# Kernel optimization log

Measured on AMD Instinct MI355X. Metric: run time of the kernel, lower is better.

Reference implementation:

```python
import jax, jax.numpy as jnp
import numpy as np

E, D_IN, H, D_OUT = 8, 6, 32, 2
B = 1048576

def setup_inputs() -> dict:
    key = jax.random.key(0)
    ks = jax.random.split(key, 11)
    s = lambda *sh: 1.0 / np.sqrt(sh[-2])  # glorot-ish scale
    x = jax.random.normal(ks[0], (B, D_IN), dtype=jnp.float32)
    # stacked expert weights
    W1 = jax.random.normal(ks[1], (E, D_IN, H), dtype=jnp.float32) * (1.0/np.sqrt(D_IN))
    b1 = jnp.zeros((E, H), dtype=jnp.float32)
    W2 = jax.random.normal(ks[2], (E, H, H), dtype=jnp.float32) * (1.0/np.sqrt(H))
    b2 = jnp.zeros((E, H), dtype=jnp.float32)
    W3 = jax.random.normal(ks[3], (E, H, D_OUT), dtype=jnp.float32) * (1.0/np.sqrt(H))
    b3 = jnp.zeros((E, D_OUT), dtype=jnp.float32)
    # gating network
    Wg1 = jax.random.normal(ks[4], (D_IN, H), dtype=jnp.float32) * (1.0/np.sqrt(D_IN))
    bg1 = jnp.zeros((H,), dtype=jnp.float32)
    Wg2 = jax.random.normal(ks[5], (H, E), dtype=jnp.float32) * (1.0/np.sqrt(H))
    bg2 = jnp.zeros((E,), dtype=jnp.float32)
    return {"x": x, "W1": W1, "b1": b1, "W2": W2, "b2": b2, "W3": W3, "b3": b3,
            "Wg1": Wg1, "bg1": bg1, "Wg2": Wg2, "bg2": bg2}

def reference(x, W1, b1, W2, b2, W3, b3, Wg1, bg1, Wg2, bg2):
    # gate: [B, E] softmax probs
    g = jax.nn.softmax(jax.nn.relu(x @ Wg1 + bg1) @ Wg2 + bg2, axis=-1)
    # all experts as batched GEMMs: h1, h2 [B, E, H]; y [B, E, 2]
    h1 = jax.nn.relu(jnp.einsum('bd,edh->beh', x, W1) + b1)
    h2 = jax.nn.relu(jnp.einsum('beh,ehk->bek', h1, W2) + b2)
    y = jnp.einsum('beh,eho->beo', h2, W3) + b3
    # gate-weighted sum over experts -> [B, 2]
    return jnp.einsum('be,beo->bo', g, y)
```

## Files before the change

kernel.cpp:

```cpp
#include <hip/hip_runtime.h>


typedef _Float16 half2_t __attribute__((ext_vector_type(2)));
typedef _Float16 half4_t __attribute__((ext_vector_type(4)));
typedef _Float16 half8_t __attribute__((ext_vector_type(8)));
typedef __fp16   fp16v2  __attribute__((ext_vector_type(2)));
typedef float  float4_t __attribute__((ext_vector_type(4)));
typedef float  float2_t __attribute__((ext_vector_type(2)));
typedef int    int2_t   __attribute__((ext_vector_type(2)));
typedef int    int4_t   __attribute__((ext_vector_type(4)));

#define MFMA_K32(A, B, C) __builtin_amdgcn_mfma_f32_16x16x32_f16((A), (B), (C), 0, 0, 0)
#define MFMA_K16(A, B, C) __builtin_amdgcn_mfma_f32_16x16x16f16((A), (B), (C), 0, 0, 0)

static constexpr int E_ = 8, DIN_ = 6, H_ = 32, EPW_ = 2;

union H8U { half2_t h2[4]; half8_t h8; int4_t i4; };
union H4U { half2_t h2[2]; half4_t h4; int2_t i2; };
union HI  { half2_t h; int i; };
union PKU { fp16v2 p; half2_t h; };
union FI  { float f; int i; };

__device__ __forceinline__ half2_t pkrtz(float a, float b) {
    PKU u; u.p = __builtin_amdgcn_cvt_pkrtz(a, b);
    return u.h;
}

__device__ __forceinline__ half2_t relu2(half2_t v) {
    const half2_t z = {(_Float16)0.0f, (_Float16)0.0f};
    return __builtin_elementwise_max(v, z);
}

__device__ __forceinline__ float bperm_f(int addr, float v) {
    FI u; u.f = v;
    u.i = __builtin_amdgcn_ds_bpermute(addr, u.i);
    return u.f;
}

__global__ __launch_bounds__(256, 2)
void moe_kernel(
    const float* __restrict__ x,  const float* __restrict__ W1, const float* __restrict__ b1,
    const float* __restrict__ W2, const float* __restrict__ b2, const float* __restrict__ W3,
    const float* __restrict__ b3, const float* __restrict__ Wg1, const float* __restrict__ bg1,
    const float* __restrict__ Wg2, const float* __restrict__ bg2,
    float* __restrict__ out, int nTiles, int tilesPerBlock)
{
    const int tid  = threadIdx.x;
    const int lane = tid & 63;
    const int t    = lane & 15;
    const int q    = lane >> 4;
    const int wv   = tid >> 6;
    const int eb   = wv * EPW_;

    __shared__ float2_t cbuf[2][4][16];

    const float L2E = 1.44269504f;

    H4U G1[2];
    #pragma unroll
    for (int f = 0; f < 2; ++f) {
        float v0 = 0.f, v1 = 0.f, v2 = 0.f, v3 = 0.f;
        if (q == 0) {
            v0 = Wg1[0 * H_ + f * 16 + t]; v1 = Wg1[1 * H_ + f * 16 + t];
            v2 = Wg1[2 * H_ + f * 16 + t]; v3 = Wg1[3 * H_ + f * 16 + t];
        } else if (q == 1) {
            v0 = Wg1[4 * H_ + f * 16 + t]; v1 = Wg1[5 * H_ + f * 16 + t];
            v2 = bg1[f * 16 + t];          v3 = 0.f;
        }
        G1[f].h2[0] = pkrtz(v0, v1); G1[f].h2[1] = pkrtz(v2, v3);
    }
    H8U G2;
    #pragma unroll
    for (int p = 0; p < 4; ++p) {
        int c0 = ((p >> 1) << 4) + q * 4 + ((p & 1) << 1);
        float v0 = (t < E_) ? Wg2[c0 * E_ + t] * L2E : 0.f;
        float v1 = (t < E_) ? Wg2[(c0 + 1) * E_ + t] * L2E : 0.f;
        G2.h2[p] = pkrtz(v0, v1);
    }

    H4U W1F[EPW_][2];
    H8U W2F[EPW_][2], W3F[EPW_], B2R[EPW_];
    #pragma unroll
    for (int j = 0; j < EPW_; ++j) {
        const int e = eb + j;
        #pragma unroll
        for (int f = 0; f < 2; ++f) {
            float v0 = 0.f, v1 = 0.f, v2 = 0.f, v3 = 0.f;
            const float* We = W1 + (size_t)e * DIN_ * H_ + f * 16 + t;
            if (q == 0)      { v0 = We[0 * H_]; v1 = We[1 * H_]; v2 = We[2 * H_]; v3 = We[3 * H_]; }
            else if (q == 1) { v0 = We[4 * H_]; v1 = We[5 * H_]; v2 = b1[e * H_ + f * 16 + t]; }
            W1F[j][f].h2[0] = pkrtz(v0, v1); W1F[j][f].h2[1] = pkrtz(v2, v3);
        }
        #pragma unroll
        for (int p = 0; p < 4; ++p) {
            int c0 = ((p >> 1) << 4) + q * 4 + ((p & 1) << 1);
            W2F[j][0].h2[p] = pkrtz(W2[(e * H_ + c0) * H_ + 0  + t], W2[(e * H_ + c0 + 1) * H_ + 0  + t]);
            W2F[j][1].h2[p] = pkrtz(W2[(e * H_ + c0) * H_ + 16 + t], W2[(e * H_ + c0 + 1) * H_ + 16 + t]);
            B2R[j].h2[p]    = pkrtz(b2[e * H_ + c0], b2[e * H_ + c0 + 1]);
            float v0 = 0.f, v1 = 0.f;
            if ((t >> 1) == e) {
                v0 = W3[(e * H_ + c0) * 2 + (t & 1)];
                v1 = W3[(e * H_ + c0 + 1) * 2 + (t & 1)];
            }
            W3F[j].h2[p] = pkrtz(v0, v1);
        }
    }

    float4_t bg2F, b3F;
    #pragma unroll
    for (int r = 0; r < 4; ++r) {
        int m = q * 4 + r;
        bg2F[r] = (m < E_) ? bg2[m] * L2E : 0.f;
        b3F[r]  = b3[m];
    }
    const float4_t zero4 = {0.f, 0.f, 0.f, 0.f};

    const int gsrc = ((((q >> 1) << 4) | t) << 2);
    const int csrc = (((wv << 4) | t) << 2);

    const int tile0 = blockIdx.x * tilesPerBlock;

    const int xo1 = (q == 0) ? 0 : 4;
    const int xo2 = (q == 0) ? 2 : 4;
    const float* xq = x + ((size_t)tile0 * 16 + t) * DIN_;
    float2_t la = {0.f, 0.f}, lb = {0.f, 0.f};
    if (tile0 < nTiles) {
        la = *(const float2_t*)(xq + xo1);
        lb = *(const float2_t*)(xq + xo2);
    }

    HI onei; onei.h = pkrtz(1.f, 0.f);
    const bool isq0 = (q == 0);

    for (int it = 0; it < tilesPerBlock; ++it) {
        const int tile = tile0 + it;
        if (tile >= nTiles) break;

        H4U ux;
        ux.h2[0] = pkrtz(la[0], la[1]);
        HI hb; hb.h = pkrtz(lb[0], lb[1]);
        HI se; se.i = isq0 ? hb.i : onei.i;
        ux.h2[1] = se.h;
        const half4_t xB = ux.h4;

        if ((it + 1) < tilesPerBlock && (tile + 1) < nTiles) {
            const float* xn = xq + (size_t)(it + 1) * 16 * DIN_;
            la = *(const float2_t*)(xn + xo1);
            lb = *(const float2_t*)(xn + xo2);
        }

        float4_t hgLo = MFMA_K16(G1[0].h4, xB, zero4);
        float4_t hgHi = MFMA_K16(G1[1].h4, xB, zero4);
        H8U uh;
        uh.h2[0] = relu2(pkrtz(hgLo[0], hgLo[1]));
        uh.h2[1] = relu2(pkrtz(hgLo[2], hgLo[3]));
        uh.h2[2] = relu2(pkrtz(hgHi[0], hgHi[1]));
        uh.h2[3] = relu2(pkrtz(hgHi[2], hgHi[3]));
        float4_t gl = MFMA_K32(G2.h8, uh.h8, bg2F);

        float ex0 = __builtin_amdgcn_exp2f(gl[0]);
        float ex1 = __builtin_amdgcn_exp2f(gl[1]);
        float ex2 = __builtin_amdgcn_exp2f(gl[2]);
        float ex3 = __builtin_amdgcn_exp2f(gl[3]);
        float s = (ex0 + ex1) + (ex2 + ex3);
        s += __shfl_xor(s, 16);
        float rs = __builtin_amdgcn_rcpf(s);
        HI pa, pb;
        pa.h = pkrtz(ex0, ex1);
        pb.h = pkrtz(ex2, ex3);
        int va = __builtin_amdgcn_ds_bpermute(gsrc, pa.i);
        int vb = __builtin_amdgcn_ds_bpermute(gsrc, pb.i);
        HI gsel; gsel.i = (q & 1) ? vb : va;
        float ga = (float)gsel.h[0];
        float gb = (float)gsel.h[1];

        float4_t Y = b3F;
        #pragma unroll
        for (int j = 0; j < EPW_; ++j) {
            float4_t lo = MFMA_K16(W1F[j][0].h4, xB, zero4);
            float4_t hi = MFMA_K16(W1F[j][1].h4, xB, zero4);
            H8U u1;
            u1.h2[0] = relu2(pkrtz(lo[0], lo[1]));
            u1.h2[1] = relu2(pkrtz(lo[2], lo[3]));
            u1.h2[2] = relu2(pkrtz(hi[0], hi[1]));
            u1.h2[3] = relu2(pkrtz(hi[2], hi[3]));
            float4_t lo2 = MFMA_K32(W2F[j][0].h8, u1.h8, zero4);
            float4_t hi2 = MFMA_K32(W2F[j][1].h8, u1.h8, zero4);
            H8U u2;
            u2.h2[0] = relu2(pkrtz(lo2[0], lo2[1]) + B2R[j].h2[0]);
            u2.h2[1] = relu2(pkrtz(lo2[2], lo2[3]) + B2R[j].h2[1]);
            u2.h2[2] = relu2(pkrtz(hi2[0], hi2[1]) + B2R[j].h2[2]);
            u2.h2[3] = relu2(pkrtz(hi2[2], hi2[3]) + B2R[j].h2[3]);
            Y = MFMA_K32(W3F[j].h8, u2.h8, Y);
        }

        float p0 = ga * Y[0] + gb * Y[2];
        float p1 = ga * Y[1] + gb * Y[3];
        p0 = bperm_f(csrc, p0);
        p1 = bperm_f(csrc, p1);

        if (lane < 16) {
            float2_t o = {p0, p1};
            cbuf[it & 1][wv][t] = o;
        }
        __syncthreads();
        if (wv == 0 && lane < 16) {
            float2_t o  = cbuf[it & 1][0][t];
            float2_t o1 = cbuf[it & 1][1][t];
            float2_t o2 = cbuf[it & 1][2][t];
            float2_t o3 = cbuf[it & 1][3][t];
            o[0] = (o[0] + o1[0] + o2[0] + o3[0]) * rs;
            o[1] = (o[1] + o1[1] + o2[1] + o3[1]) * rs;
            *(float2_t*)(out + ((size_t)tile * 16 + t) * 2) = o;
        }
    }
}

extern "C" void kernel_launch(void* const* d_in, const int* in_sizes, int n_in,
                              void* d_out, int out_size, void* d_ws, size_t ws_size,
                              hipStream_t stream) {
    const float* x   = (const float*)d_in[0];
    const float* W1  = (const float*)d_in[1];
    const float* b1  = (const float*)d_in[2];
    const float* W2  = (const float*)d_in[3];
    const float* b2  = (const float*)d_in[4];
    const float* W3  = (const float*)d_in[5];
    const float* b3  = (const float*)d_in[6];
    const float* Wg1 = (const float*)d_in[7];
    const float* bg1 = (const float*)d_in[8];
    const float* Wg2 = (const float*)d_in[9];
    const float* bg2 = (const float*)d_in[10];
    float* out = (float*)d_out;

    const int B      = in_sizes[0] / DIN_;
    const int nTiles = (B + 15) / 16;
    const int blocks = 2048;
    const int tpb    = (nTiles + blocks - 1) / blocks;

    moe_kernel<<<blocks, 256, 0, stream>>>(x, W1, b1, W2, b2, W3, b3,
                                           Wg1, bg1, Wg2, bg2, out, nTiles, tpb);
}
```

Before: 155.3 us.

## Switch MoE tile pipeline to 32x32x16 MFMA with 32-row tiles

Reworks every GEMM stage (gate and expert layers) from 16x16 MFMA shapes to 32x32x16 f16 MFMAs that process 32 batch rows per tile. The fragment layouts, the gate softmax exchange (now a cross-half shuffle) and the output reduction are rewritten to match. The b2 bias moves to packed shared memory and the b3 bias is folded in after gating. The aim is fewer MFMA and conversion instructions per row and less per-tile sync overhead. The cost is larger accumulators, more register pressure, and half as many blocks.

After: 163.2 us. 5.1% more time.

```diff
diff --git a/kernel.cpp b/kernel.cpp
--- a/kernel.cpp
+++ b/kernel.cpp
@@ -2,24 +2,19 @@
 
 
 typedef _Float16 half2_t __attribute__((ext_vector_type(2)));
-typedef _Float16 half4_t __attribute__((ext_vector_type(4)));
 typedef _Float16 half8_t __attribute__((ext_vector_type(8)));
 typedef __fp16   fp16v2  __attribute__((ext_vector_type(2)));
-typedef float  float4_t __attribute__((ext_vector_type(4)));
-typedef float  float2_t __attribute__((ext_vector_type(2)));
-typedef int    int2_t   __attribute__((ext_vector_type(2)));
-typedef int    int4_t   __attribute__((ext_vector_type(4)));
-
-#define MFMA_K32(A, B, C) __builtin_amdgcn_mfma_f32_16x16x32_f16((A), (B), (C), 0, 0, 0)
-#define MFMA_K16(A, B, C) __builtin_amdgcn_mfma_f32_16x16x16f16((A), (B), (C), 0, 0, 0)
+typedef float  float2_t  __attribute__((ext_vector_type(2)));
+typedef float  float16_t __attribute__((ext_vector_type(16)));
+typedef int    int4_t    __attribute__((ext_vector_type(4)));
+
+#define MFMA32(A, B, C) __builtin_amdgcn_mfma_f32_32x32x16_f16((A), (B), (C), 0, 0, 0)
 
 static constexpr int E_ = 8, DIN_ = 6, H_ = 32, EPW_ = 2;
 
 union H8U { half2_t h2[4]; half8_t h8; int4_t i4; };
-union H4U { half2_t h2[2]; half4_t h4; int2_t i2; };
 union HI  { half2_t h; int i; };
 union PKU { fp16v2 p; half2_t h; };
-union FI  { float f; int i; };
 
 __device__ __forceinline__ half2_t pkrtz(float a, float b) {
     PKU u; u.p = __builtin_amdgcn_cvt_pkrtz(a, b);
@@ -31,13 +26,11 @@
     return __builtin_elementwise_max(v, z);
 }
 
-__device__ __forceinline__ float bperm_f(int addr, float v) {
-    FI u; u.f = v;
-    u.i = __builtin_amdgcn_ds_bpermute(addr, u.i);
-    return u.f;
-}
-
-__global__ __launch_bounds__(256, 2)
+__device__ __forceinline__ int sigma(int p, int h, int j) {
+    return (j & 3) + 8 * ((j >> 2) + 2 * p) + 4 * h;
+}
+
+__global__ __launch_bounds__(256)
 void moe_kernel(
     const float* __restrict__ x,  const float* __restrict__ W1, const float* __restrict__ b1,
     const float* __restrict__ W2, const float* __restrict__ b2, const float* __restrict__ W3,
@@ -47,171 +40,195 @@
 {
     const int tid  = threadIdx.x;
     const int lane = tid & 63;
-    const int t    = lane & 15;
-    const int q    = lane >> 4;
+    const int t32  = lane & 31;
+    const int h    = lane >> 5;
     const int wv   = tid >> 6;
     const int eb   = wv * EPW_;
 
-    __shared__ float2_t cbuf[2][4][16];
+    __shared__ int      b2pk[128];
+    __shared__ float2_t cbuf[2][4][32];
 
     const float L2E = 1.44269504f;
 
-    H4U G1[2];
-    #pragma unroll
-    for (int f = 0; f < 2; ++f) {
-        float v0 = 0.f, v1 = 0.f, v2 = 0.f, v3 = 0.f;
-        if (q == 0) {
-            v0 = Wg1[0 * H_ + f * 16 + t]; v1 = Wg1[1 * H_ + f * 16 + t];
-            v2 = Wg1[2 * H_ + f * 16 + t]; v3 = Wg1[3 * H_ + f * 16 + t];
-        } else if (q == 1) {
-            v0 = Wg1[4 * H_ + f * 16 + t]; v1 = Wg1[5 * H_ + f * 16 + t];
-            v2 = bg1[f * 16 + t];          v3 = 0.f;
-        }
-        G1[f].h2[0] = pkrtz(v0, v1); G1[f].h2[1] = pkrtz(v2, v3);
-    }
-    H8U G2;
-    #pragma unroll
-    for (int p = 0; p < 4; ++p) {
-        int c0 = ((p >> 1) << 4) + q * 4 + ((p & 1) << 1);
-        float v0 = (t < E_) ? Wg2[c0 * E_ + t] * L2E : 0.f;
-        float v1 = (t < E_) ? Wg2[(c0 + 1) * E_ + t] * L2E : 0.f;
-        G2.h2[p] = pkrtz(v0, v1);
-    }
-
-    H4U W1F[EPW_][2];
-    H8U W2F[EPW_][2], W3F[EPW_], B2R[EPW_];
-    #pragma unroll
-    for (int j = 0; j < EPW_; ++j) {
-        const int e = eb + j;
-        #pragma unroll
-        for (int f = 0; f < 2; ++f) {
-            float v0 = 0.f, v1 = 0.f, v2 = 0.f, v3 = 0.f;
-            const float* We = W1 + (size_t)e * DIN_ * H_ + f * 16 + t;
-            if (q == 0)      { v0 = We[0 * H_]; v1 = We[1 * H_]; v2 = We[2 * H_]; v3 = We[3 * H_]; }
-            else if (q == 1) { v0 = We[4 * H_]; v1 = We[5 * H_]; v2 = b1[e * H_ + f * 16 + t]; }
-            W1F[j][f].h2[0] = pkrtz(v0, v1); W1F[j][f].h2[1] = pkrtz(v2, v3);
-        }
-        #pragma unroll
-        for (int p = 0; p < 4; ++p) {
-            int c0 = ((p >> 1) << 4) + q * 4 + ((p & 1) << 1);
-            W2F[j][0].h2[p] = pkrtz(W2[(e * H_ + c0) * H_ + 0  + t], W2[(e * H_ + c0 + 1) * H_ + 0  + t]);
-            W2F[j][1].h2[p] = pkrtz(W2[(e * H_ + c0) * H_ + 16 + t], W2[(e * H_ + c0 + 1) * H_ + 16 + t]);
-            B2R[j].h2[p]    = pkrtz(b2[e * H_ + c0], b2[e * H_ + c0 + 1]);
+    if (tid < 128) {
+        int e = tid >> 4, hh = (tid >> 3) & 1, s = tid & 7;
+        int r0 = ((2 * s) & 3) + 8 * (s >> 1) + 4 * hh;
+        HI u; u.h = pkrtz(b2[e * H_ + r0], b2[e * H_ + r0 + 1]);
+        b2pk[tid] = u.i;
+    }
+    __syncthreads();
+
+    const int m = t32;
+
+    H8U G1;
+    #pragma unroll
+    for (int r = 0; r < 4; ++r) {
+        int j0 = 2 * r, j1 = 2 * r + 1;
+        float v0 = 0.f, v1 = 0.f;
+        if (h == 0) {
+            v0 = (j0 < DIN_) ? Wg1[j0 * H_ + m] : ((j0 == DIN_) ? bg1[m] : 0.f);
+            v1 = (j1 < DIN_) ? Wg1[j1 * H_ + m] : ((j1 == DIN_) ? bg1[m] : 0.f);
+        }
+        G1.h2[r] = pkrtz(v0, v1);
+    }
+    H8U Gg2[2];
+    #pragma unroll
+    for (int p = 0; p < 2; ++p)
+        #pragma unroll
+        for (int r = 0; r < 4; ++r) {
+            int c0 = sigma(p, h, 2 * r);
+            float v0 = (m < E_) ? Wg2[c0 * E_ + m] * L2E : 0.f;
+            float v1 = (m < E_) ? Wg2[(c0 + 1) * E_ + m] * L2E : 0.f;
+            Gg2[p].h2[r] = pkrtz(v0, v1);
+        }
+
+    H8U A1[EPW_], A2[EPW_][2], A3[EPW_][2];
+    #pragma unroll
+    for (int jx = 0; jx < EPW_; ++jx) {
+        const int e = eb + jx;
+        #pragma unroll
+        for (int r = 0; r < 4; ++r) {
+            int j0 = 2 * r, j1 = 2 * r + 1;
             float v0 = 0.f, v1 = 0.f;
-            if ((t >> 1) == e) {
-                v0 = W3[(e * H_ + c0) * 2 + (t & 1)];
-                v1 = W3[(e * H_ + c0 + 1) * 2 + (t & 1)];
-            }
-            W3F[j].h2[p] = pkrtz(v0, v1);
-        }
-    }
-
-    float4_t bg2F, b3F;
+            if (h == 0) {
+                v0 = (j0 < DIN_) ? W1[(e * DIN_ + j0) * H_ + m] : ((j0 == DIN_) ? b1[e * H_ + m] : 0.f);
+                v1 = (j1 < DIN_) ? W1[(e * DIN_ + j1) * H_ + m] : ((j1 == DIN_) ? b1[e * H_ + m] : 0.f);
+            }
+            A1[jx].h2[r] = pkrtz(v0, v1);
+        }
+        #pragma unroll
+        for (int p = 0; p < 2; ++p)
+            #pragma unroll
+            for (int r = 0; r < 4; ++r) {
+                int c0 = sigma(p, h, 2 * r);
+                A2[jx][p].h2[r] = pkrtz(W2[(e * H_ + c0) * H_ + m], W2[(e * H_ + c0 + 1) * H_ + m]);
+            }
+        const bool mine = (m >> 1) == e;
+        const int  o    = m & 1;
+        #pragma unroll
+        for (int p = 0; p < 2; ++p)
+            #pragma unroll
+            for (int r = 0; r < 4; ++r) {
+                int c0 = sigma(p, h, 2 * r);
+                float v0 = mine ? W3[(e * H_ + c0) * 2 + o] : 0.f;
+                float v1 = mine ? W3[(e * H_ + c0 + 1) * 2 + o] : 0.f;
+                A3[jx][p].h2[r] = pkrtz(v0, v1);
+            }
+    }
+
+    float bg2F[4], b3A[4], b3B[4];
     #pragma unroll
     for (int r = 0; r < 4; ++r) {
-        int m = q * 4 + r;
-        bg2F[r] = (m < E_) ? bg2[m] * L2E : 0.f;
-        b3F[r]  = b3[m];
-    }
-    const float4_t zero4 = {0.f, 0.f, 0.f, 0.f};
-
-    const int gsrc = ((((q >> 1) << 4) | t) << 2);
-    const int csrc = (((wv << 4) | t) << 2);
+        bg2F[r] = bg2[r + 4 * h] * L2E;
+        b3A[r]  = b3[4 * h + r];
+        b3B[r]  = b3[8 + 4 * h + r];
+    }
+    const float16_t zero16 = {0.f,0.f,0.f,0.f, 0.f,0.f,0.f,0.f, 0.f,0.f,0.f,0.f, 0.f,0.f,0.f,0.f};
 
     const int tile0 = blockIdx.x * tilesPerBlock;
 
-    const int xo1 = (q == 0) ? 0 : 4;
-    const int xo2 = (q == 0) ? 2 : 4;
-    const float* xq = x + ((size_t)tile0 * 16 + t) * DIN_;
-    float2_t la = {0.f, 0.f}, lb = {0.f, 0.f};
+    const float* xq = x + ((size_t)tile0 * 32 + t32) * DIN_;
+    float2_t la = {0.f, 0.f}, lb = {0.f, 0.f}, lc = {0.f, 0.f};
     if (tile0 < nTiles) {
-        la = *(const float2_t*)(xq + xo1);
-        lb = *(const float2_t*)(xq + xo2);
-    }
-
-    HI onei; onei.h = pkrtz(1.f, 0.f);
-    const bool isq0 = (q == 0);
+        la = *(const float2_t*)(xq + 0);
+        lb = *(const float2_t*)(xq + 2);
+        lc = *(const float2_t*)(xq + 4);
+    }
+    HI one0; one0.h = pkrtz(1.f, 0.f);
 
     for (int it = 0; it < tilesPerBlock; ++it) {
         const int tile = tile0 + it;
         if (tile >= nTiles) break;
 
-        H4U ux;
+        H8U ux;
         ux.h2[0] = pkrtz(la[0], la[1]);
-        HI hb; hb.h = pkrtz(lb[0], lb[1]);
-        HI se; se.i = isq0 ? hb.i : onei.i;
-        ux.h2[1] = se.h;
-        const half4_t xB = ux.h4;
+        ux.h2[1] = pkrtz(lb[0], lb[1]);
+        ux.h2[2] = pkrtz(lc[0], lc[1]);
+        ux.h2[3] = one0.h;
+        const half8_t xB = ux.h8;
 
         if ((it + 1) < tilesPerBlock && (tile + 1) < nTiles) {
-            const float* xn = xq + (size_t)(it + 1) * 16 * DIN_;
-            la = *(const float2_t*)(xn + xo1);
-            lb = *(const float2_t*)(xn + xo2);
-        }
-
-        float4_t hgLo = MFMA_K16(G1[0].h4, xB, zero4);
-        float4_t hgHi = MFMA_K16(G1[1].h4, xB, zero4);
-        H8U uh;
-        uh.h2[0] = relu2(pkrtz(hgLo[0], hgLo[1]));
-        uh.h2[1] = relu2(pkrtz(hgLo[2], hgLo[3]));
-        uh.h2[2] = relu2(pkrtz(hgHi[0], hgHi[1]));
-        uh.h2[3] = relu2(pkrtz(hgHi[2], hgHi[3]));
-        float4_t gl = MFMA_K32(G2.h8, uh.h8, bg2F);
-
-        float ex0 = __builtin_amdgcn_exp2f(gl[0]);
-        float ex1 = __builtin_amdgcn_exp2f(gl[1]);
-        float ex2 = __builtin_amdgcn_exp2f(gl[2]);
-        float ex3 = __builtin_amdgcn_exp2f(gl[3]);
+            const float* xn = xq + (size_t)(it + 1) * 32 * DIN_;
+            la = *(const float2_t*)(xn + 0);
+            lb = *(const float2_t*)(xn + 2);
+            lc = *(const float2_t*)(xn + 4);
+        }
+
+        float16_t Cg = MFMA32(G1.h8, xB, zero16);
+        H8U bg0, bg1v;
+        #pragma unroll
+        for (int r = 0; r < 4; ++r) {
+            bg0.h2[r]  = relu2(pkrtz(Cg[2 * r], Cg[2 * r + 1]));
+            bg1v.h2[r] = relu2(pkrtz(Cg[8 + 2 * r], Cg[9 + 2 * r]));
+        }
+        float16_t Cg2 = MFMA32(Gg2[0].h8, bg0.h8, zero16);
+        Cg2 = MFMA32(Gg2[1].h8, bg1v.h8, Cg2);
+
+        float ex0 = __builtin_amdgcn_exp2f(Cg2[0] + bg2F[0]);
+        float ex1 = __builtin_amdgcn_exp2f(Cg2[1] + bg2F[1]);
+        float ex2 = __builtin_amdgcn_exp2f(Cg2[2] + bg2F[2]);
+        float ex3 = __builtin_amdgcn_exp2f(Cg2[3] + bg2F[3]);
         float s = (ex0 + ex1) + (ex2 + ex3);
-        s += __shfl_xor(s, 16);
+        s += __shfl_xor(s, 32);
         float rs = __builtin_amdgcn_rcpf(s);
-        HI pa, pb;
+        HI pa, pb, xpa, xpb, eA, eB;
         pa.h = pkrtz(ex0, ex1);
         pb.h = pkrtz(ex2, ex3);
-        int va = __builtin_amdgcn_ds_bpermute(gsrc, pa.i);
-        int vb = __builtin_amdgcn_ds_bpermute(gsrc, pb.i);
-        HI gsel; gsel.i = (q & 1) ? vb : va;
-        float ga = (float)gsel.h[0];
-        float gb = (float)gsel.h[1];
-
-        float4_t Y = b3F;
-        #pragma unroll
-        for (int j = 0; j < EPW_; ++j) {
-            float4_t lo = MFMA_K16(W1F[j][0].h4, xB, zero4);
-            float4_t hi = MFMA_K16(W1F[j][1].h4, xB, zero4);
-            H8U u1;
-            u1.h2[0] = relu2(pkrtz(lo[0], lo[1]));
-            u1.h2[1] = relu2(pkrtz(lo[2], lo[3]));
-            u1.h2[2] = relu2(pkrtz(hi[0], hi[1]));
-            u1.h2[3] = relu2(pkrtz(hi[2], hi[3]));
-            float4_t lo2 = MFMA_K32(W2F[j][0].h8, u1.h8, zero4);
-            float4_t hi2 = MFMA_K32(W2F[j][1].h8, u1.h8, zero4);
-            H8U u2;
-            u2.h2[0] = relu2(pkrtz(lo2[0], lo2[1]) + B2R[j].h2[0]);
-            u2.h2[1] = relu2(pkrtz(lo2[2], lo2[3]) + B2R[j].h2[1]);
-            u2.h2[2] = relu2(pkrtz(hi2[0], hi2[1]) + B2R[j].h2[2]);
-            u2.h2[3] = relu2(pkrtz(hi2[2], hi2[3]) + B2R[j].h2[3]);
-            Y = MFMA_K32(W3F[j].h8, u2.h8, Y);
-        }
-
-        float p0 = ga * Y[0] + gb * Y[2];
-        float p1 = ga * Y[1] + gb * Y[3];
-        p0 = bperm_f(csrc, p0);
-        p1 = bperm_f(csrc, p1);
-
-        if (lane < 16) {
+        xpa.i = __shfl_xor(pa.i, 32);
+        xpb.i = __shfl_xor(pb.i, 32);
+        eA.i = h ? xpb.i : pa.i;
+        eB.i = h ? pb.i  : xpa.i;
+        float gA0 = (float)eA.h[0], gA1 = (float)eA.h[1];
+        float gB0 = (float)eB.h[0], gB1 = (float)eB.h[1];
+
+        float16_t Y = zero16;
+        #pragma unroll
+        for (int jx = 0; jx < EPW_; ++jx) {
+            float16_t C1 = MFMA32(A1[jx].h8, xB, zero16);
+            H8U u0, u1;
+            #pragma unroll
+            for (int r = 0; r < 4; ++r) {
+                u0.h2[r] = relu2(pkrtz(C1[2 * r], C1[2 * r + 1]));
+                u1.h2[r] = relu2(pkrtz(C1[8 + 2 * r], C1[9 + 2 * r]));
+            }
+            float16_t C2 = MFMA32(A2[jx][0].h8, u0.h8, zero16);
+            C2 = MFMA32(A2[jx][1].h8, u1.h8, C2);
+            H8U ua, ub;
+            const int base = (eb + jx) * 16 + h * 8;
+            ua.i4 = *(const int4_t*)&b2pk[base];
+            ub.i4 = *(const int4_t*)&b2pk[base + 4];
+            H8U q0, q1;
+            #pragma unroll
+            for (int r = 0; r < 4; ++r) {
+                q0.h2[r] = relu2(pkrtz(C2[2 * r], C2[2 * r + 1]) + ua.h2[r]);
+                q1.h2[r] = relu2(pkrtz(C2[8 + 2 * r], C2[9 + 2 * r]) + ub.h2[r]);
+            }
+            Y = MFMA32(A3[jx][0].h8, q0.h8, Y);
+            Y = MFMA32(A3[jx][1].h8, q1.h8, Y);
+        }
+
+        float p0 = gA0 * Y[0] + gA1 * Y[2] + gB0 * Y[4] + gB1 * Y[6];
+        float p1 = gA0 * Y[1] + gA1 * Y[3] + gB0 * Y[5] + gB1 * Y[7];
+        if (wv == 0) {
+            p0 += gA0 * b3A[0] + gA1 * b3A[2] + gB0 * b3B[0] + gB1 * b3B[2];
+            p1 += gA0 * b3A[1] + gA1 * b3A[3] + gB0 * b3B[1] + gB1 * b3B[3];
+        }
+        p0 += __shfl_xor(p0, 32);
+        p1 += __shfl_xor(p1, 32);
+
+        if (lane < 32) {
             float2_t o = {p0, p1};
-            cbuf[it & 1][wv][t] = o;
+            cbuf[it & 1][wv][t32] = o;
         }
         __syncthreads();
-        if (wv == 0 && lane < 16) {
-            float2_t o  = cbuf[it & 1][0][t];
-            float2_t o1 = cbuf[it & 1][1][t];
-            float2_t o2 = cbuf[it & 1][2][t];
-            float2_t o3 = cbuf[it & 1][3][t];
+        if (wv == 0 && lane < 32) {
+            float2_t o  = cbuf[it & 1][0][t32];
+            float2_t o1 = cbuf[it & 1][1][t32];
+            float2_t o2 = cbuf[it & 1][2][t32];
+            float2_t o3 = cbuf[it & 1][3][t32];
             o[0] = (o[0] + o1[0] + o2[0] + o3[0]) * rs;
             o[1] = (o[1] + o1[1] + o2[1] + o3[1]) * rs;
-            *(float2_t*)(out + ((size_t)tile * 16 + t) * 2) = o;
+            *(float2_t*)(out + ((size_t)tile * 32 + t32) * 2) = o;
         }
     }
 }
@@ -233,8 +250,8 @@
     float* out = (float*)d_out;
 
     const int B      = in_sizes[0] / DIN_;
-    const int nTiles = (B + 15) / 16;
-    const int blocks = 2048;
+    const int nTiles = (B + 31) / 32;
+    const int blocks = 1024;
     const int tpb    = (nTiles + blocks - 1) / blocks;
 
     moe_kernel<<<blocks, 256, 0, stream>>>(x, W1, b1, W2, b2, W3, b3,
```

## Process two tiles per iteration to interleave independent MFMA chains

Applied to the files above, without the earlier changes.

The per-tile loop is unrolled by two. The gating and expert MFMA chains of the two tiles are interleaved so their latencies can overlap, and the two results share one shared-memory reduction and one __syncthreads. The minimum-occupancy hint is also removed from the launch bounds, which lets the compiler use more registers for the doubled live state. The risks are higher register pressure and lower occupancy, and, if tilesPerBlock is odd, redundant work and writes to a tile that belongs to the next block.

Result: slower. 166.4 us (+7.1%).

```diff
diff --git a/kernel.cpp b/kernel.cpp
--- a/kernel.cpp
+++ b/kernel.cpp
@@ -37,7 +37,7 @@
     return u.f;
 }
 
-__global__ __launch_bounds__(256, 2)
+__global__ __launch_bounds__(256)
 void moe_kernel(
     const float* __restrict__ x,  const float* __restrict__ W1, const float* __restrict__ b1,
     const float* __restrict__ W2, const float* __restrict__ b2, const float* __restrict__ W3,
@@ -52,7 +52,7 @@
     const int wv   = tid >> 6;
     const int eb   = wv * EPW_;
 
-    __shared__ float2_t cbuf[2][4][16];
+    __shared__ float2_t cbuf[2][2][4][16];
 
     const float L2E = 1.44269504f;
 
@@ -123,95 +123,150 @@
     const int xo1 = (q == 0) ? 0 : 4;
     const int xo2 = (q == 0) ? 2 : 4;
     const float* xq = x + ((size_t)tile0 * 16 + t) * DIN_;
-    float2_t la = {0.f, 0.f}, lb = {0.f, 0.f};
-    if (tile0 < nTiles) {
-        la = *(const float2_t*)(xq + xo1);
-        lb = *(const float2_t*)(xq + xo2);
-    }
+    const int strideT = 16 * DIN_;
+
+    float2_t laA = {0.f,0.f}, lbA = {0.f,0.f}, laB = {0.f,0.f}, lbB = {0.f,0.f};
+    if (tile0 < nTiles)     { laA = *(const float2_t*)(xq + xo1);           lbA = *(const float2_t*)(xq + xo2); }
+    if (tile0 + 1 < nTiles) { laB = *(const float2_t*)(xq + strideT + xo1); lbB = *(const float2_t*)(xq + strideT + xo2); }
 
     HI onei; onei.h = pkrtz(1.f, 0.f);
     const bool isq0 = (q == 0);
 
-    for (int it = 0; it < tilesPerBlock; ++it) {
-        const int tile = tile0 + it;
-        if (tile >= nTiles) break;
-
-        H4U ux;
-        ux.h2[0] = pkrtz(la[0], la[1]);
-        HI hb; hb.h = pkrtz(lb[0], lb[1]);
-        HI se; se.i = isq0 ? hb.i : onei.i;
-        ux.h2[1] = se.h;
-        const half4_t xB = ux.h4;
-
-        if ((it + 1) < tilesPerBlock && (tile + 1) < nTiles) {
-            const float* xn = xq + (size_t)(it + 1) * 16 * DIN_;
-            la = *(const float2_t*)(xn + xo1);
-            lb = *(const float2_t*)(xn + xo2);
-        }
-
-        float4_t hgLo = MFMA_K16(G1[0].h4, xB, zero4);
-        float4_t hgHi = MFMA_K16(G1[1].h4, xB, zero4);
-        H8U uh;
-        uh.h2[0] = relu2(pkrtz(hgLo[0], hgLo[1]));
-        uh.h2[1] = relu2(pkrtz(hgLo[2], hgLo[3]));
-        uh.h2[2] = relu2(pkrtz(hgHi[0], hgHi[1]));
-        uh.h2[3] = relu2(pkrtz(hgHi[2], hgHi[3]));
-        float4_t gl = MFMA_K32(G2.h8, uh.h8, bg2F);
-
-        float ex0 = __builtin_amdgcn_exp2f(gl[0]);
-        float ex1 = __builtin_amdgcn_exp2f(gl[1]);
-        float ex2 = __builtin_amdgcn_exp2f(gl[2]);
-        float ex3 = __builtin_amdgcn_exp2f(gl[3]);
-        float s = (ex0 + ex1) + (ex2 + ex3);
-        s += __shfl_xor(s, 16);
-        float rs = __builtin_amdgcn_rcpf(s);
-        HI pa, pb;
-        pa.h = pkrtz(ex0, ex1);
-        pb.h = pkrtz(ex2, ex3);
-        int va = __builtin_amdgcn_ds_bpermute(gsrc, pa.i);
-        int vb = __builtin_amdgcn_ds_bpermute(gsrc, pb.i);
-        HI gsel; gsel.i = (q & 1) ? vb : va;
-        float ga = (float)gsel.h[0];
-        float gb = (float)gsel.h[1];
-
-        float4_t Y = b3F;
+    for (int it = 0; it < tilesPerBlock; it += 2) {
+        const int tA = tile0 + it;
+        if (tA >= nTiles) break;
+        const int  tB   = tA + 1;
+        const bool hasB = (tB < nTiles);
+
+        H4U uxA, uxB;
+        {
+            uxA.h2[0] = pkrtz(laA[0], laA[1]);
+            HI hb; hb.h = pkrtz(lbA[0], lbA[1]);
+            HI se; se.i = isq0 ? hb.i : onei.i;
+            uxA.h2[1] = se.h;
+            uxB.h2[0] = pkrtz(laB[0], laB[1]);
+            HI hb2; hb2.h = pkrtz(lbB[0], lbB[1]);
+            HI se2; se2.i = isq0 ? hb2.i : onei.i;
+            uxB.h2[1] = se2.h;
+        }
+        const half4_t xBA = uxA.h4;
+        const half4_t xBB = uxB.h4;
+
+        if ((it + 2) < tilesPerBlock) {
+            const float* xn = xq + (size_t)(it + 2) * strideT;
+            if (tA + 2 < nTiles) { laA = *(const float2_t*)(xn + xo1);           lbA = *(const float2_t*)(xn + xo2); }
+            if (tA + 3 < nTiles) { laB = *(const float2_t*)(xn + strideT + xo1); lbB = *(const float2_t*)(xn + strideT + xo2); }
+        }
+
+        float4_t glA, glB;
+        {
+            float4_t hgLo = MFMA_K16(G1[0].h4, xBA, zero4);
+            float4_t hgHi = MFMA_K16(G1[1].h4, xBA, zero4);
+            float4_t hgLo2 = MFMA_K16(G1[0].h4, xBB, zero4);
+            float4_t hgHi2 = MFMA_K16(G1[1].h4, xBB, zero4);
+            H8U uh, uh2;
+            uh.h2[0] = relu2(pkrtz(hgLo[0], hgLo[1]));
+            uh.h2[1] = relu2(pkrtz(hgLo[2], hgLo[3]));
+            uh.h2[2] = relu2(pkrtz(hgHi[0], hgHi[1]));
+            uh.h2[3] = relu2(pkrtz(hgHi[2], hgHi[3]));
+            uh2.h2[0] = relu2(pkrtz(hgLo2[0], hgLo2[1]));
+            uh2.h2[1] = relu2(pkrtz(hgLo2[2], hgLo2[3]));
+            uh2.h2[2] = relu2(pkrtz(hgHi2[0], hgHi2[1]));
+            uh2.h2[3] = relu2(pkrtz(hgHi2[2], hgHi2[3]));
+            glA = MFMA_K32(G2.h8, uh.h8, bg2F);
+            glB = MFMA_K32(G2.h8, uh2.h8, bg2F);
+        }
+
+        float exA0 = __builtin_amdgcn_exp2f(glA[0]);
+        float exA1 = __builtin_amdgcn_exp2f(glA[1]);
+        float exA2 = __builtin_amdgcn_exp2f(glA[2]);
+        float exA3 = __builtin_amdgcn_exp2f(glA[3]);
+        float exB0 = __builtin_amdgcn_exp2f(glB[0]);
+        float exB1 = __builtin_amdgcn_exp2f(glB[1]);
+        float exB2 = __builtin_amdgcn_exp2f(glB[2]);
+        float exB3 = __builtin_amdgcn_exp2f(glB[3]);
+        float sA = (exA0 + exA1) + (exA2 + exA3);
+        float sB = (exB0 + exB1) + (exB2 + exB3);
+        sA += __shfl_xor(sA, 16);
+        sB += __shfl_xor(sB, 16);
+        float rsA = __builtin_amdgcn_rcpf(sA);
+        float rsB = __builtin_amdgcn_rcpf(sB);
+        HI paA, pbA, paB, pbB;
+        paA.h = pkrtz(exA0, exA1);  pbA.h = pkrtz(exA2, exA3);
+        paB.h = pkrtz(exB0, exB1);  pbB.h = pkrtz(exB2, exB3);
+        int vaA = __builtin_amdgcn_ds_bpermute(gsrc, paA.i);
+        int vbA = __builtin_amdgcn_ds_bpermute(gsrc, pbA.i);
+        int vaB = __builtin_amdgcn_ds_bpermute(gsrc, paB.i);
+        int vbB = __builtin_amdgcn_ds_bpermute(gsrc, pbB.i);
+        HI gsA; gsA.i = (q & 1) ? vbA : vaA;
+        HI gsB; gsB.i = (q & 1) ? vbB : vaB;
+        float gaA = (float)gsA.h[0], gbA = (float)gsA.h[1];
+        float gaB = (float)gsB.h[0], gbB = (float)gsB.h[1];
+
+        float4_t YA = b3F, YB = b3F;
         #pragma unroll
         for (int j = 0; j < EPW_; ++j) {
-            float4_t lo = MFMA_K16(W1F[j][0].h4, xB, zero4);
-            float4_t hi = MFMA_K16(W1F[j][1].h4, xB, zero4);
-            H8U u1;
-            u1.h2[0] = relu2(pkrtz(lo[0], lo[1]));
-            u1.h2[1] = relu2(pkrtz(lo[2], lo[3]));
-            u1.h2[2] = relu2(pkrtz(hi[0], hi[1]));
-            u1.h2[3] = relu2(pkrtz(hi[2], hi[3]));
-            float4_t lo2 = MFMA_K32(W2F[j][0].h8, u1.h8, zero4);
-            float4_t hi2 = MFMA_K32(W2F[j][1].h8, u1.h8, zero4);
-            H8U u2;
-            u2.h2[0] = relu2(pkrtz(lo2[0], lo2[1]) + B2R[j].h2[0]);
-            u2.h2[1] = relu2(pkrtz(lo2[2], lo2[3]) + B2R[j].h2[1]);
-            u2.h2[2] = relu2(pkrtz(hi2[0], hi2[1]) + B2R[j].h2[2]);
-            u2.h2[3] = relu2(pkrtz(hi2[2], hi2[3]) + B2R[j].h2[3]);
-            Y = MFMA_K32(W3F[j].h8, u2.h8, Y);
-        }
-
-        float p0 = ga * Y[0] + gb * Y[2];
-        float p1 = ga * Y[1] + gb * Y[3];
-        p0 = bperm_f(csrc, p0);
-        p1 = bperm_f(csrc, p1);
-
-        if (lane < 16) {
-            float2_t o = {p0, p1};
-            cbuf[it & 1][wv][t] = o;
+            float4_t loA = MFMA_K16(W1F[j][0].h4, xBA, zero4);
+            float4_t hiA = MFMA_K16(W1F[j][1].h4, xBA, zero4);
+            float4_t loB = MFMA_K16(W1F[j][0].h4, xBB, zero4);
+            float4_t hiB = MFMA_K16(W1F[j][1].h4, xBB, zero4);
+            H8U u1A, u1B;
+            u1A.h2[0] = relu2(pkrtz(loA[0], loA[1]));
+            u1A.h2[1] = relu2(pkrtz(loA[2], loA[3]));
+            u1A.h2[2] = relu2(pkrtz(hiA[0], hiA[1]));
+            u1A.h2[3] = relu2(pkrtz(hiA[2], hiA[3]));
+            u1B.h2[0] = relu2(pkrtz(loB[0], loB[1]));
+            u1B.h2[1] = relu2(pkrtz(loB[2], loB[3]));
+            u1B.h2[2] = relu2(pkrtz(hiB[0], hiB[1]));
+            u1B.h2[3] = relu2(pkrtz(hiB[2], hiB[3]));
+            float4_t lo2A = MFMA_K32(W2F[j][0].h8, u1A.h8, zero4);
+            float4_t hi2A = MFMA_K32(W2F[j][1].h8, u1A.h8, zero4);
+            float4_t lo2B = MFMA_K32(W2F[j][0].h8, u1B.h8, zero4);
+            float4_t hi2B = MFMA_K32(W2F[j][1].h8, u1B.h8, zero4);
+            H8U u2A, u2B;
+            u2A.h2[0] = relu2(pkrtz(lo2A[0], lo2A[1]) + B2R[j].h2[0]);
+            u2A.h2[1] = relu2(pkrtz(lo2A[2], lo2A[3]) + B2R[j].h2[1]);
+            u2A.h2[2] = relu2(pkrtz(hi2A[0], hi2A[1]) + B2R[j].h2[2]);
+            u2A.h2[3] = relu2(pkrtz(hi2A[2], hi2A[3]) + B2R[j].h2[3]);
+            u2B.h2[0] = relu2(pkrtz(lo2B[0], lo2B[1]) + B2R[j].h2[0]);
+            u2B.h2[1] = relu2(pkrtz(lo2B[2], lo2B[3]) + B2R[j].h2[1]);
+            u2B.h2[2] = relu2(pkrtz(hi2B[0], hi2B[1]) + B2R[j].h2[2]);
+            u2B.h2[3] = relu2(pkrtz(hi2B[2], hi2B[3]) + B2R[j].h2[3]);
+            YA = MFMA_K32(W3F[j].h8, u2A.h8, YA);
+            YB = MFMA_K32(W3F[j].h8, u2B.h8, YB);
+        }
+
+        float pA0 = gaA * YA[0] + gbA * YA[2];
+        float pA1 = gaA * YA[1] + gbA * YA[3];
+        float pB0 = gaB * YB[0] + gbB * YB[2];
+        float pB1 = gaB * YB[1] + gbB * YB[3];
+        pA0 = bperm_f(csrc, pA0);
+        pA1 = bperm_f(csrc, pA1);
+        pB0 = bperm_f(csrc, pB0);
+        pB1 = bperm_f(csrc, pB1);
+
+        const int par = (it >> 1) & 1;
+        if (lane < 32) {
+            const int sel = lane >> 4;
+            float2_t o;
+            o[0] = sel ? pB0 : pA0;
+            o[1] = sel ? pB1 : pA1;
+            cbuf[par][sel][wv][t] = o;
         }
         __syncthreads();
-        if (wv == 0 && lane < 16) {
-            float2_t o  = cbuf[it & 1][0][t];
-            float2_t o1 = cbuf[it & 1][1][t];
-            float2_t o2 = cbuf[it & 1][2][t];
-            float2_t o3 = cbuf[it & 1][3][t];
-            o[0] = (o[0] + o1[0] + o2[0] + o3[0]) * rs;
-            o[1] = (o[1] + o1[1] + o2[1] + o3[1]) * rs;
-            *(float2_t*)(out + ((size_t)tile * 16 + t) * 2) = o;
+        if (wv == 0 && lane < 32) {
+            const int sel = lane >> 4;
+            if (sel == 0 || hasB) {
+                float2_t o  = cbuf[par][sel][0][t];
+                float2_t o1 = cbuf[par][sel][1][t];
+                float2_t o2 = cbuf[par][sel][2][t];
+                float2_t o3 = cbuf[par][sel][3][t];
+                const float rss = sel ? rsB : rsA;
+                const int   tt  = sel ? tB : tA;
+                o[0] = (o[0] + o1[0] + o2[0] + o3[0]) * rss;
+                o[1] = (o[1] + o1[1] + o2[1] + o3[1]) * rss;
+                *(float2_t*)(out + ((size_t)tt * 16 + t) * 2) = o;
+            }
         }
     }
 }
```

## Split experts across two kernel passes with independent waves, no block sync

Applied to the files above, without the earlier changes.

The old work split had four waves per block each handle two experts of the same tile and combine through shared memory with a __syncthreads every tile. The new version launches two kernels, each covering four experts. Every wave owns its own tiles, so partial sums are reduced with cross-lane shuffles and the block barrier goes away. Pass 0 computes the gate softmax and stores normalized fp16 probabilities in the workspace. Pass 1 reads those probabilities and the partial outputs back and accumulates, which adds extra global traffic, a second launch, and x being read twice.

Result: slower. 185.5 us (+19.4%).

```diff
diff --git a/kernel.cpp b/kernel.cpp
--- a/kernel.cpp
+++ b/kernel.cpp
@@ -13,7 +13,7 @@
 #define MFMA_K32(A, B, C) __builtin_amdgcn_mfma_f32_16x16x32_f16((A), (B), (C), 0, 0, 0)
 #define MFMA_K16(A, B, C) __builtin_amdgcn_mfma_f32_16x16x16f16((A), (B), (C), 0, 0, 0)
 
-static constexpr int E_ = 8, DIN_ = 6, H_ = 32, EPW_ = 2;
+static constexpr int E_ = 8, DIN_ = 6, H_ = 32, EPK_ = 4;
 
 union H8U { half2_t h2[4]; half8_t h8; int4_t i4; };
 union H4U { half2_t h2[2]; half4_t h4; int2_t i2; };
@@ -31,57 +31,52 @@
     return __builtin_elementwise_max(v, z);
 }
 
-__device__ __forceinline__ float bperm_f(int addr, float v) {
-    FI u; u.f = v;
-    u.i = __builtin_amdgcn_ds_bpermute(addr, u.i);
-    return u.f;
-}
-
-__global__ __launch_bounds__(256, 2)
-void moe_kernel(
+template<int PASS>
+__global__ __launch_bounds__(256)
+void moe_pass(
     const float* __restrict__ x,  const float* __restrict__ W1, const float* __restrict__ b1,
     const float* __restrict__ W2, const float* __restrict__ b2, const float* __restrict__ W3,
     const float* __restrict__ b3, const float* __restrict__ Wg1, const float* __restrict__ bg1,
     const float* __restrict__ Wg2, const float* __restrict__ bg2,
-    float* __restrict__ out, int nTiles, int tilesPerBlock)
+    float* __restrict__ out, int* __restrict__ gws, int Btok, int nTiles, int tilesPerWave)
 {
     const int tid  = threadIdx.x;
     const int lane = tid & 63;
     const int t    = lane & 15;
     const int q    = lane >> 4;
-    const int wv   = tid >> 6;
-    const int eb   = wv * EPW_;
-
-    __shared__ float2_t cbuf[2][4][16];
+    const int wid  = (int)((blockIdx.x * blockDim.x + tid) >> 6);
+    const int eb   = PASS * EPK_;
 
     const float L2E = 1.44269504f;
 
     H4U G1[2];
+    H8U G2;
+    if constexpr (PASS == 0) {
+        #pragma unroll
+        for (int f = 0; f < 2; ++f) {
+            float v0 = 0.f, v1 = 0.f, v2 = 0.f, v3 = 0.f;
+            if (q == 0) {
+                v0 = Wg1[0 * H_ + f * 16 + t]; v1 = Wg1[1 * H_ + f * 16 + t];
+                v2 = Wg1[2 * H_ + f * 16 + t]; v3 = Wg1[3 * H_ + f * 16 + t];
+            } else if (q == 1) {
+                v0 = Wg1[4 * H_ + f * 16 + t]; v1 = Wg1[5 * H_ + f * 16 + t];
+                v2 = bg1[f * 16 + t];          v3 = 0.f;
+            }
+            G1[f].h2[0] = pkrtz(v0, v1); G1[f].h2[1] = pkrtz(v2, v3);
+        }
+        #pragma unroll
+        for (int p = 0; p < 4; ++p) {
+            int c0 = ((p >> 1) << 4) + q * 4 + ((p & 1) << 1);
+            float v0 = (t < E_) ? Wg2[c0 * E_ + t] * L2E : 0.f;
+            float v1 = (t < E_) ? Wg2[(c0 + 1) * E_ + t] * L2E : 0.f;
+            G2.h2[p] = pkrtz(v0, v1);
+        }
+    }
+
+    H4U W1F[EPK_][2];
+    H8U W2F[EPK_][2], W3F[EPK_], B2R[EPK_];
     #pragma unroll
-    for (int f = 0; f < 2; ++f) {
-        float v0 = 0.f, v1 = 0.f, v2 = 0.f, v3 = 0.f;
-        if (q == 0) {
-            v0 = Wg1[0 * H_ + f * 16 + t]; v1 = Wg1[1 * H_ + f * 16 + t];
-            v2 = Wg1[2 * H_ + f * 16 + t]; v3 = Wg1[3 * H_ + f * 16 + t];
-        } else if (q == 1) {
-            v0 = Wg1[4 * H_ + f * 16 + t]; v1 = Wg1[5 * H_ + f * 16 + t];
-            v2 = bg1[f * 16 + t];          v3 = 0.f;
-        }
-        G1[f].h2[0] = pkrtz(v0, v1); G1[f].h2[1] = pkrtz(v2, v3);
-    }
-    H8U G2;
-    #pragma unroll
-    for (int p = 0; p < 4; ++p) {
-        int c0 = ((p >> 1) << 4) + q * 4 + ((p & 1) << 1);
-        float v0 = (t < E_) ? Wg2[c0 * E_ + t] * L2E : 0.f;
-        float v1 = (t < E_) ? Wg2[(c0 + 1) * E_ + t] * L2E : 0.f;
-        G2.h2[p] = pkrtz(v0, v1);
-    }
-
-    H4U W1F[EPW_][2];
-    H8U W2F[EPW_][2], W3F[EPW_], B2R[EPW_];
-    #pragma unroll
-    for (int j = 0; j < EPW_; ++j) {
+    for (int j = 0; j < EPK_; ++j) {
         const int e = eb + j;
         #pragma unroll
         for (int f = 0; f < 2; ++f) {
@@ -111,30 +106,33 @@
     for (int r = 0; r < 4; ++r) {
         int m = q * 4 + r;
         bg2F[r] = (m < E_) ? bg2[m] * L2E : 0.f;
-        b3F[r]  = b3[m];
+        b3F[r]  = ((q >> 1) == PASS) ? b3[m] : 0.f;
     }
     const float4_t zero4 = {0.f, 0.f, 0.f, 0.f};
 
-    const int gsrc = ((((q >> 1) << 4) | t) << 2);
-    const int csrc = (((wv << 4) | t) << 2);
-
-    const int tile0 = blockIdx.x * tilesPerBlock;
+    const int tile0 = wid * tilesPerWave;
 
     const int xo1 = (q == 0) ? 0 : 4;
     const int xo2 = (q == 0) ? 2 : 4;
     const float* xq = x + ((size_t)tile0 * 16 + t) * DIN_;
+    const int strideT = 16 * DIN_;
+
     float2_t la = {0.f, 0.f}, lb = {0.f, 0.f};
+    int gcur = 0;
     if (tile0 < nTiles) {
         la = *(const float2_t*)(xq + xo1);
         lb = *(const float2_t*)(xq + xo2);
+        if constexpr (PASS == 1)
+            gcur = gws[(q & 1) * Btok + tile0 * 16 + t];
     }
 
     HI onei; onei.h = pkrtz(1.f, 0.f);
     const bool isq0 = (q == 0);
 
-    for (int it = 0; it < tilesPerBlock; ++it) {
+    for (int it = 0; it < tilesPerWave; ++it) {
         const int tile = tile0 + it;
         if (tile >= nTiles) break;
+        const int tok = tile * 16 + t;
 
         H4U ux;
         ux.h2[0] = pkrtz(la[0], la[1]);
@@ -143,40 +141,59 @@
         ux.h2[1] = se.h;
         const half4_t xB = ux.h4;
 
-        if ((it + 1) < tilesPerBlock && (tile + 1) < nTiles) {
-            const float* xn = xq + (size_t)(it + 1) * 16 * DIN_;
+        float2_t oprev = {0.f, 0.f};
+        if constexpr (PASS == 1) {
+            if (lane < 16) oprev = *(const float2_t*)(out + (size_t)tok * 2);
+        }
+
+        int gnext = 0;
+        if ((it + 1) < tilesPerWave && (tile + 1) < nTiles) {
+            const float* xn = xq + (size_t)(it + 1) * strideT;
             la = *(const float2_t*)(xn + xo1);
             lb = *(const float2_t*)(xn + xo2);
-        }
-
-        float4_t hgLo = MFMA_K16(G1[0].h4, xB, zero4);
-        float4_t hgHi = MFMA_K16(G1[1].h4, xB, zero4);
-        H8U uh;
-        uh.h2[0] = relu2(pkrtz(hgLo[0], hgLo[1]));
-        uh.h2[1] = relu2(pkrtz(hgLo[2], hgLo[3]));
-        uh.h2[2] = relu2(pkrtz(hgHi[0], hgHi[1]));
-        uh.h2[3] = relu2(pkrtz(hgHi[2], hgHi[3]));
-        float4_t gl = MFMA_K32(G2.h8, uh.h8, bg2F);
-
-        float ex0 = __builtin_amdgcn_exp2f(gl[0]);
-        float ex1 = __builtin_amdgcn_exp2f(gl[1]);
-        float ex2 = __builtin_amdgcn_exp2f(gl[2]);
-        float ex3 = __builtin_amdgcn_exp2f(gl[3]);
-        float s = (ex0 + ex1) + (ex2 + ex3);
-        s += __shfl_xor(s, 16);
-        float rs = __builtin_amdgcn_rcpf(s);
-        HI pa, pb;
-        pa.h = pkrtz(ex0, ex1);
-        pb.h = pkrtz(ex2, ex3);
-        int va = __builtin_amdgcn_ds_bpermute(gsrc, pa.i);
-        int vb = __builtin_amdgcn_ds_bpermute(gsrc, pb.i);
-        HI gsel; gsel.i = (q & 1) ? vb : va;
-        float ga = (float)gsel.h[0];
-        float gb = (float)gsel.h[1];
+            if constexpr (PASS == 1)
+                gnext = gws[(q & 1) * Btok + (tile + 1) * 16 + t];
+        }
+
+        float ga, gb;
+        if constexpr (PASS == 0) {
+            float4_t hgLo = MFMA_K16(G1[0].h4, xB, zero4);
+            float4_t hgHi = MFMA_K16(G1[1].h4, xB, zero4);
+            H8U uh;
+            uh.h2[0] = relu2(pkrtz(hgLo[0], hgLo[1]));
+            uh.h2[1] = relu2(pkrtz(hgLo[2], hgLo[3]));
+            uh.h2[2] = relu2(pkrtz(hgHi[0], hgHi[1]));
+            uh.h2[3] = relu2(pkrtz(hgHi[2], hgHi[3]));
+            float4_t gl = MFMA_K32(G2.h8, uh.h8, bg2F);
+            float ex0 = __builtin_amdgcn_exp2f(gl[0]);
+            float ex1 = __builtin_amdgcn_exp2f(gl[1]);
+            float ex2 = __builtin_amdgcn_exp2f(gl[2]);
+            float ex3 = __builtin_amdgcn_exp2f(gl[3]);
+            float s = (ex0 + ex1) + (ex2 + ex3);
+            s += __shfl_xor(s, 16);
+            float rs = __builtin_amdgcn_rcpf(s);
+            HI pa, pb;
+            pa.h = pkrtz(ex0 * rs, ex1 * rs);
+            pb.h = pkrtz(ex2 * rs, ex3 * rs);
+            if (q == 1) {
+                gws[tok]        = pa.i;
+                gws[Btok + tok] = pb.i;
+            }
+            int va = __builtin_amdgcn_ds_bpermute(t << 2, pa.i);
+            int vb = __builtin_amdgcn_ds_bpermute(t << 2, pb.i);
+            HI gsel; gsel.i = (q & 1) ? vb : va;
+            ga = (float)gsel.h[0];
+            gb = (float)gsel.h[1];
+        } else {
+            HI gsel; gsel.i = gcur;
+            ga = (float)gsel.h[0];
+            gb = (float)gsel.h[1];
+            gcur = gnext;
+        }
 
         float4_t Y = b3F;
         #pragma unroll
-        for (int j = 0; j < EPW_; ++j) {
+        for (int j = 0; j < EPK_; ++j) {
             float4_t lo = MFMA_K16(W1F[j][0].h4, xB, zero4);
             float4_t hi = MFMA_K16(W1F[j][1].h4, xB, zero4);
             H8U u1;
@@ -196,22 +213,15 @@
 
         float p0 = ga * Y[0] + gb * Y[2];
         float p1 = ga * Y[1] + gb * Y[3];
-        p0 = bperm_f(csrc, p0);
-        p1 = bperm_f(csrc, p1);
-
+        p0 += __shfl_xor(p0, 16);
+        p0 += __shfl_xor(p0, 32);
+        p1 += __shfl_xor(p1, 16);
+        p1 += __shfl_xor(p1, 32);
         if (lane < 16) {
-            float2_t o = {p0, p1};
-            cbuf[it & 1][wv][t] = o;
-        }
-        __syncthreads();
-        if (wv == 0 && lane < 16) {
-            float2_t o  = cbuf[it & 1][0][t];
-            float2_t o1 = cbuf[it & 1][1][t];
-            float2_t o2 = cbuf[it & 1][2][t];
-            float2_t o3 = cbuf[it & 1][3][t];
-            o[0] = (o[0] + o1[0] + o2[0] + o3[0]) * rs;
-            o[1] = (o[1] + o1[1] + o2[1] + o3[1]) * rs;
-            *(float2_t*)(out + ((size_t)tile * 16 + t) * 2) = o;
+            float2_t o;
+            o[0] = p0 + oprev[0];
+            o[1] = p1 + oprev[1];
+            *(float2_t*)(out + (size_t)tok * 2) = o;
         }
     }
 }
@@ -231,12 +241,16 @@
     const float* Wg2 = (const float*)d_in[9];
     const float* bg2 = (const float*)d_in[10];
     float* out = (float*)d_out;
+    int*   gws = (int*)d_ws;
 
     const int B      = in_sizes[0] / DIN_;
     const int nTiles = (B + 15) / 16;
     const int blocks = 2048;
-    const int tpb    = (nTiles + blocks - 1) / blocks;
-
-    moe_kernel<<<blocks, 256, 0, stream>>>(x, W1, b1, W2, b2, W3, b3,
-                                           Wg1, bg1, Wg2, bg2, out, nTiles, tpb);
-}
+    const int nWaves = blocks * (256 / 64);
+    const int tpw    = (nTiles + nWaves - 1) / nWaves;
+
+    moe_pass<0><<<blocks, 256, 0, stream>>>(x, W1, b1, W2, b2, W3, b3,
+                                            Wg1, bg1, Wg2, bg2, out, gws, B, nTiles, tpw);
+    moe_pass<1><<<blocks, 256, 0, stream>>>(x, W1, b1, W2, b2, W3, b3,
+                                            Wg1, bg1, Wg2, bg2, out, gws, B, nTiles, tpw);
+}
```
